# Kernel optimization log

Hardware: AMD Instinct MI355X
Metric: run time of the kernel (lower is better)

Reference implementation:

```python
import jax, jax.numpy as jnp
import numpy as np

N = 8192
D_IN = 60
NUM_CLASSES = 10


def _xavier(key, out_f, in_f):
    limit = float(np.sqrt(6.0 / (in_f + out_f)))
    return jax.random.uniform(key, (out_f, in_f), jnp.float32, -limit, limit)


def setup_inputs() -> dict:
    key = jax.random.key(0)
    ks = jax.random.split(key, 10)
    return {
        "x": jax.random.normal(ks[0], (N, D_IN), jnp.float32),
        "fc1_w": _xavier(ks[1], 32, 60),
        "fc1_b": jnp.zeros((32,), jnp.float32),
        "fc2_w": _xavier(ks[2], 16, 32),
        "fc2_b": jnp.zeros((16,), jnp.float32),
        "fc3_w": _xavier(ks[3], 8, 60),
        "fc3_b": jnp.zeros((8,), jnp.float32),
        "fc6_w": _xavier(ks[4], NUM_CLASSES, 8),
        "fc6_b": jnp.zeros((NUM_CLASSES,), jnp.float32),
        "temp": jnp.float32(1.0) + 0.1 * jax.random.truncated_normal(ks[5], -2.0, 2.0, (), jnp.float32),
        "theta": jnp.float32(1.0) + 0.1 * jax.random.truncated_normal(ks[6], -2.0, 2.0, (), jnp.float32),
    }


def _pairwise_sq_dist(z):
    # z: [N, d] -> [N, N] squared euclidean distances, clamped at 0
    sq = jnp.sum(z * z, axis=1)  # [N]
    dist = sq[:, None] + sq[None, :] - 2.0 * (z @ z.T)
    return jnp.maximum(dist, 0.0)


def reference(x, fc1_w, fc1_b, fc2_w, fc2_b, fc3_w, fc3_b, fc6_w, fc6_b, temp, theta):
    net = x @ fc1_w.T + fc1_b           # [N, 32]
    net = net @ fc2_w.T + fc2_b         # [N, 16]
    A = -_pairwise_sq_dist(net)         # [N, N]
    A = jax.nn.sigmoid(temp * A + theta)
    # A * (1 - I) + I == set diagonal to 1
    A = jnp.fill_diagonal(A, 1.0, inplace=False)
    A = A / jnp.sum(A, axis=1, keepdims=True)
    h = A @ x                           # [N, 60] dense graph aggregation
    h = h @ fc3_w.T + fc3_b             # [N, 8]
    return jax.nn.softmax(h @ fc6_w.T + fc6_b, axis=1)  # [N, num_classes]
```

## Files before the change

kernel.cpp:

```cpp
#include <hip/hip_runtime.h>
#include <math.h>

#define NROWS 8192
#define DIN   60
#define DZ    16
#define NC    10

#define LOG2E 1.4426950408889634f

#define RB      128
#define CJ      512
#define NRB     (NROWS / RB)
#define NCH     (NROWS / CJ)
#define WAVES   4
#define REGIONS (NRB * WAVES)

#define CHPAD (NROWS * 64 + 1024)

typedef short    bf16x8 __attribute__((ext_vector_type(8)));
typedef float    f32x4  __attribute__((ext_vector_type(4)));
typedef float    f32x16 __attribute__((ext_vector_type(16)));
typedef unsigned u32x2  __attribute__((ext_vector_type(2)));

__device__ __forceinline__ unsigned int bfr(float f) {
    return (__float_as_uint(f) + 0x8000u) >> 16;
}

__global__ __launch_bounds__(64) void k1_all(
    const float* __restrict__ x,
    const float* __restrict__ w1, const float* __restrict__ b1,
    const float* __restrict__ w2, const float* __restrict__ b2,
    const float* __restrict__ temp_p, const float* __restrict__ theta_p,
    unsigned short* __restrict__ zb, float* __restrict__ bbf,
    unsigned short* __restrict__ xT)
{
    int i = blockIdx.x * 64 + threadIdx.x;

    float xr[DIN];
    const float4* xp = reinterpret_cast<const float4*>(x + (size_t)i * DIN);
    #pragma unroll
    for (int c = 0; c < 15; ++c) {
        float4 v = xp[c];
        xr[c*4+0] = v.x; xr[c*4+1] = v.y; xr[c*4+2] = v.z; xr[c*4+3] = v.w;
    }

    float n1[32];
    #pragma unroll
    for (int o = 0; o < 32; ++o) {
        float acc = b1[o];
        #pragma unroll
        for (int k = 0; k < DIN; ++k) acc = fmaf(w1[o*DIN+k], xr[k], acc);
        n1[o] = acc;
    }

    float z[DZ];
    float sq = 0.0f;
    #pragma unroll
    for (int u = 0; u < DZ; ++u) {
        float acc = b2[u];
        #pragma unroll
        for (int o = 0; o < 32; ++o) acc = fmaf(w2[u*32+o], n1[o], acc);
        z[u] = acc;
        sq = fmaf(acc, acc, sq);
    }

    float temp  = *temp_p;
    float theta = *theta_p;
    float s = sqrtf(2.0f * temp * LOG2E);

    unsigned int p[8];
    #pragma unroll
    for (int u = 0; u < 8; ++u) {
        unsigned int lo = bfr(z[2*u]   * s);
        unsigned int hi = bfr(z[2*u+1] * s);
        p[u] = lo | (hi << 16);
    }
    uint4* dst = reinterpret_cast<uint4*>(zb + (size_t)i * 16);
    dst[0] = make_uint4(p[0], p[1], p[2], p[3]);
    dst[1] = make_uint4(p[4], p[5], p[6], p[7]);

    bbf[i] = LOG2E * fmaf(temp, sq, -0.5f * theta);

    #pragma unroll
    for (int c = 0; c < DIN; ++c)
        xT[(size_t)c * NROWS + i] = (unsigned short)bfr(xr[c]);
    xT[(size_t)60 * NROWS + i] = 0x3F80;
    xT[(size_t)61 * NROWS + i] = 0;
    xT[(size_t)62 * NROWS + i] = 0;
    xT[(size_t)63 * NROWS + i] = 0;
}

__global__ __launch_bounds__(256) void k2_mfma(
    const unsigned short* __restrict__ zb, const float* __restrict__ bbf,
    const unsigned short* __restrict__ xT, const float* __restrict__ theta_p,
    float* __restrict__ hacc)
{
    const int tid  = threadIdx.x;
    const int lane = tid & 63, wave = tid >> 6;
    const int ic = lane & 31;
    const int h  = lane >> 5;
    const int rb = blockIdx.x & (NRB - 1);
    const int ch = blockIdx.x >> 6;
    const int it = rb * RB + wave * 32;
    const int j0 = ch * CJ;

    bf16x8 zbi = *reinterpret_cast<const bf16x8*>(zb + (size_t)(it + ic) * 16 + h * 8);
    const float bi = bbf[it + ic];
    const float nclamp = -(*theta_p) * LOG2E;

    const int  dd   = ic - 4 * h;
    const bool dl   = (dd >= 0) && ((dd & 7) < 4);
    const int  dreg = dl ? (((dd >> 3) << 2) | (dd & 3)) : -1;

    f32x16 z16;
    #pragma unroll
    for (int k = 0; k < 16; ++k) z16[k] = 0.0f;
    f32x16 H0 = z16, H1 = z16;

    for (int jb = 0; jb < CJ / 32; ++jb) {
        const int jt = j0 + jb * 32;
        bf16x8 za = *reinterpret_cast<const bf16x8*>(zb + (size_t)(jt + ic) * 16 + h * 8);
        f32x16 S = __builtin_amdgcn_mfma_f32_32x32x16_bf16(za, zbi, z16, 0, 0, 0);

        const bool dblk = (it == jt);
        unsigned pk[8];
        #pragma unroll
        for (int u = 0; u < 4; ++u) {
            f32x4 bj = *reinterpret_cast<const f32x4*>(bbf + jt + u * 8 + 4 * h);
            unsigned ur[4];
            #pragma unroll
            for (int r = 0; r < 4; ++r) {
                const int reg = u * 4 + r;
                float n = (bi + bj[r]) - S[reg];
                n = fmaxf(n, nclamp);
                float P = __builtin_amdgcn_rcpf(1.0f + __builtin_amdgcn_exp2f(n));
                if (dblk && reg == dreg) P = 0.0f;
                ur[r] = __float_as_uint(P) + 0x8000u;
            }
            pk[u*2 + 0] = (ur[0] >> 16) | (ur[1] & 0xFFFF0000u);
            pk[u*2 + 1] = (ur[2] >> 16) | (ur[3] & 0xFFFF0000u);
        }

        u32x2 sA = __builtin_amdgcn_permlane32_swap(pk[0], pk[2], false, false);
        u32x2 sB = __builtin_amdgcn_permlane32_swap(pk[1], pk[3], false, false);
        u32x2 sC = __builtin_amdgcn_permlane32_swap(pk[4], pk[6], false, false);
        u32x2 sD = __builtin_amdgcn_permlane32_swap(pk[5], pk[7], false, false);
        union { unsigned u[4]; bf16x8 v; } pa0, pa1;
        pa0.u[0] = sA[0]; pa0.u[1] = sB[0]; pa0.u[2] = sA[1]; pa0.u[3] = sB[1];
        pa1.u[0] = sC[0]; pa1.u[1] = sD[0]; pa1.u[2] = sC[1]; pa1.u[3] = sD[1];

        {
            bf16x8 xb0 = *reinterpret_cast<const bf16x8*>(
                xT + (size_t)(ic) * NROWS + jt + h*8);
            bf16x8 xb1 = *reinterpret_cast<const bf16x8*>(
                xT + (size_t)(ic) * NROWS + jt + 16 + h*8);
            H0 = __builtin_amdgcn_mfma_f32_32x32x16_bf16(pa0.v, xb0, H0, 0, 0, 0);
            H0 = __builtin_amdgcn_mfma_f32_32x32x16_bf16(pa1.v, xb1, H0, 0, 0, 0);
        }
        {
            bf16x8 xb0 = *reinterpret_cast<const bf16x8*>(
                xT + (size_t)(32 + ic) * NROWS + jt + h*8);
            bf16x8 xb1 = *reinterpret_cast<const bf16x8*>(
                xT + (size_t)(32 + ic) * NROWS + jt + 16 + h*8);
            H1 = __builtin_amdgcn_mfma_f32_32x32x16_bf16(pa0.v, xb0, H1, 0, 0, 0);
            H1 = __builtin_amdgcn_mfma_f32_32x32x16_bf16(pa1.v, xb1, H1, 0, 0, 0);
        }
    }

    const int region = rb * WAVES + wave;
    float* outp = hacc + (size_t)ch * CHPAD + (size_t)region * 2048;
    #pragma unroll
    for (int reg = 0; reg < 16; ++reg)
        outp[reg * 64 + lane] = H0[reg];
    #pragma unroll
    for (int reg = 0; reg < 16; ++reg)
        outp[(16 + reg) * 64 + lane] = H1[reg];
}

__global__ __launch_bounds__(256) void k3_fused(
    const float* __restrict__ hacc,
    const float* __restrict__ x,
    const float* __restrict__ w3, const float* __restrict__ b3,
    const float* __restrict__ w6, const float* __restrict__ b6,
    float* __restrict__ out)
{
    __shared__ float sh[16][64];

    const int tid    = threadIdx.x;
    const int b      = blockIdx.x;
    const int region = b >> 1, sub = b & 1;

    {
        const int nt   = tid >> 7;
        const int foff = (tid & 127) * 4;
        const int rr   = foff >> 6;
        const int lane = foff & 63;
        const size_t base = (size_t)region * 2048 + nt * 1024 + sub * 512 + foff;

        float4 s = make_float4(0.0f, 0.0f, 0.0f, 0.0f);
        #pragma unroll 4
        for (int cc = 0; cc < NCH; ++cc) {
            int ch = (cc + b) & (NCH - 1);
            float4 v = *reinterpret_cast<const float4*>(
                hacc + (size_t)ch * CHPAD + base);
            s.x += v.x; s.y += v.y; s.z += v.z; s.w += v.w;
        }
        const int il  = (rr & 3) + 8 * (rr >> 2) + 4 * (lane >> 5);
        const int col = nt * 32 + (lane & 31);
        *reinterpret_cast<float4*>(&sh[il][col]) = s;
    }
    __syncthreads();

    if (tid < 16) {
        const int row = region * 32 + sub * 16 + tid;
        const float* hi = sh[tid];
        const float* xi = x + (size_t)row * DIN;

        float rd = __builtin_amdgcn_rcpf(hi[60] + 1.0f);

        float h[DIN];
        #pragma unroll
        for (int k = 0; k < DIN; ++k) h[k] = (hi[k] + xi[k]) * rd;

        float g[8];
        #pragma unroll
        for (int o = 0; o < 8; ++o) {
            float a = b3[o];
            #pragma unroll
            for (int k = 0; k < DIN; ++k) a = fmaf(w3[o*DIN+k], h[k], a);
            g[o] = a;
        }

        float l[NC];
        float m = -3.0e38f;
        #pragma unroll
        for (int c = 0; c < NC; ++c) {
            float a = b6[c];
            #pragma unroll
            for (int o = 0; o < 8; ++o) a = fmaf(w6[c*8+o], g[o], a);
            l[c] = a;
            m = fmaxf(m, a);
        }
        float e[NC];
        float sum = 0.0f;
        #pragma unroll
        for (int c = 0; c < NC; ++c) {
            e[c] = __builtin_amdgcn_exp2f((l[c] - m) * LOG2E);
            sum += e[c];
        }
        float rsum = __builtin_amdgcn_rcpf(sum);
        #pragma unroll
        for (int c = 0; c < NC; ++c) out[(size_t)row * NC + c] = e[c] * rsum;
    }
}

extern "C" void kernel_launch(void* const* d_in, const int* in_sizes, int n_in,
                              void* d_out, int out_size, void* d_ws, size_t ws_size,
                              hipStream_t stream)
{
    const float* x     = (const float*)d_in[0];
    const float* w1    = (const float*)d_in[1];
    const float* b1    = (const float*)d_in[2];
    const float* w2    = (const float*)d_in[3];
    const float* b2    = (const float*)d_in[4];
    const float* w3    = (const float*)d_in[5];
    const float* b3    = (const float*)d_in[6];
    const float* w6    = (const float*)d_in[7];
    const float* b6    = (const float*)d_in[8];
    const float* temp  = (const float*)d_in[9];
    const float* theta = (const float*)d_in[10];
    float* out = (float*)d_out;

    char* p = (char*)d_ws;
    unsigned short* zbuf = (unsigned short*)p;  p += (size_t)NROWS * 16 * 2;
    float*          bbf  = (float*)p;           p += (size_t)NROWS * 4;
    unsigned short* xT   = (unsigned short*)p;  p += (size_t)64 * NROWS * 2;
    float*          hacc = (float*)p;

    k1_all  <<<NROWS / 64, 64, 0, stream>>>(x, w1, b1, w2, b2, temp, theta, zbuf, bbf, xT);
    k2_mfma <<<NRB * NCH, 256, 0, stream>>>(zbuf, bbf, xT, theta, hacc);
    k3_fused<<<REGIONS * 2, 256, 0, stream>>>(hacc, x, w3, b3, w6, b6, out);
}
```

Measured before the change: 179.2 us.

## Replace per-chunk partial buffers with atomic accumulation into a single output buffer

k2 now reduces its 16 column-chunk partials with float atomic adds straight into one 8192x64 buffer, zeroed by a memset, instead of writing 16 separate partial slabs that k3 then summed. k3 becomes a simple per-row head kernel reading the finished sums. This removes about 32 MB of partial writes and reads plus the reduction pass. In exchange it adds atomic contention and a memset, and the summation order is no longer deterministic.

```diff
diff --git a/kernel.cpp b/kernel.cpp
--- a/kernel.cpp
+++ b/kernel.cpp
@@ -13,9 +13,6 @@
 #define NRB     (NROWS / RB)
 #define NCH     (NROWS / CJ)
 #define WAVES   4
-#define REGIONS (NRB * WAVES)
-
-#define CHPAD (NROWS * 64 + 1024)
 
 typedef short    bf16x8 __attribute__((ext_vector_type(8)));
 typedef float    f32x4  __attribute__((ext_vector_type(4)));
@@ -93,7 +90,7 @@
 __global__ __launch_bounds__(256) void k2_mfma(
     const unsigned short* __restrict__ zb, const float* __restrict__ bbf,
     const unsigned short* __restrict__ xT, const float* __restrict__ theta_p,
-    float* __restrict__ hacc)
+    float* __restrict__ hfin)
 {
     const int tid  = threadIdx.x;
     const int lane = tid & 63, wave = tid >> 6;
@@ -167,91 +164,61 @@
         }
     }
 
-    const int region = rb * WAVES + wave;
-    float* outp = hacc + (size_t)ch * CHPAD + (size_t)region * 2048;
-    #pragma unroll
-    for (int reg = 0; reg < 16; ++reg)
-        outp[reg * 64 + lane] = H0[reg];
-    #pragma unroll
-    for (int reg = 0; reg < 16; ++reg)
-        outp[(16 + reg) * 64 + lane] = H1[reg];
-}
-
-__global__ __launch_bounds__(256) void k3_fused(
-    const float* __restrict__ hacc,
+    #pragma unroll
+    for (int reg = 0; reg < 16; ++reg) {
+        const int row = it + (reg & 3) + 8 * (reg >> 2) + 4 * h;
+        unsafeAtomicAdd(hfin + (size_t)row * 64 + ic,      H0[reg]);
+        unsafeAtomicAdd(hfin + (size_t)row * 64 + 32 + ic, H1[reg]);
+    }
+}
+
+__global__ __launch_bounds__(64) void k3_head(
     const float* __restrict__ x,
     const float* __restrict__ w3, const float* __restrict__ b3,
     const float* __restrict__ w6, const float* __restrict__ b6,
+    const float* __restrict__ hfin,
     float* __restrict__ out)
 {
-    __shared__ float sh[16][64];
-
-    const int tid    = threadIdx.x;
-    const int b      = blockIdx.x;
-    const int region = b >> 1, sub = b & 1;
-
-    {
-        const int nt   = tid >> 7;
-        const int foff = (tid & 127) * 4;
-        const int rr   = foff >> 6;
-        const int lane = foff & 63;
-        const size_t base = (size_t)region * 2048 + nt * 1024 + sub * 512 + foff;
-
-        float4 s = make_float4(0.0f, 0.0f, 0.0f, 0.0f);
-        #pragma unroll 4
-        for (int cc = 0; cc < NCH; ++cc) {
-            int ch = (cc + b) & (NCH - 1);
-            float4 v = *reinterpret_cast<const float4*>(
-                hacc + (size_t)ch * CHPAD + base);
-            s.x += v.x; s.y += v.y; s.z += v.z; s.w += v.w;
-        }
-        const int il  = (rr & 3) + 8 * (rr >> 2) + 4 * (lane >> 5);
-        const int col = nt * 32 + (lane & 31);
-        *reinterpret_cast<float4*>(&sh[il][col]) = s;
-    }
-    __syncthreads();
-
-    if (tid < 16) {
-        const int row = region * 32 + sub * 16 + tid;
-        const float* hi = sh[tid];
-        const float* xi = x + (size_t)row * DIN;
-
-        float rd = __builtin_amdgcn_rcpf(hi[60] + 1.0f);
-
-        float h[DIN];
-        #pragma unroll
-        for (int k = 0; k < DIN; ++k) h[k] = (hi[k] + xi[k]) * rd;
-
-        float g[8];
-        #pragma unroll
-        for (int o = 0; o < 8; ++o) {
-            float a = b3[o];
-            #pragma unroll
-            for (int k = 0; k < DIN; ++k) a = fmaf(w3[o*DIN+k], h[k], a);
-            g[o] = a;
-        }
-
-        float l[NC];
-        float m = -3.0e38f;
-        #pragma unroll
-        for (int c = 0; c < NC; ++c) {
-            float a = b6[c];
-            #pragma unroll
-            for (int o = 0; o < 8; ++o) a = fmaf(w6[c*8+o], g[o], a);
-            l[c] = a;
-            m = fmaxf(m, a);
-        }
-        float e[NC];
-        float sum = 0.0f;
-        #pragma unroll
-        for (int c = 0; c < NC; ++c) {
-            e[c] = __builtin_amdgcn_exp2f((l[c] - m) * LOG2E);
-            sum += e[c];
-        }
-        float rsum = __builtin_amdgcn_rcpf(sum);
-        #pragma unroll
-        for (int c = 0; c < NC; ++c) out[(size_t)row * NC + c] = e[c] * rsum;
-    }
+    int i = blockIdx.x * 64 + threadIdx.x;
+
+    const float* hi = hfin + (size_t)i * 64;
+    const float* xi = x + (size_t)i * DIN;
+
+    float rd = __builtin_amdgcn_rcpf(hi[60] + 1.0f);
+
+    float h[DIN];
+    #pragma unroll
+    for (int k = 0; k < DIN; ++k) h[k] = (hi[k] + xi[k]) * rd;
+
+    float g[8];
+    #pragma unroll
+    for (int o = 0; o < 8; ++o) {
+        float a = b3[o];
+        #pragma unroll
+        for (int k = 0; k < DIN; ++k) a = fmaf(w3[o*DIN+k], h[k], a);
+        g[o] = a;
+    }
+
+    float l[NC];
+    float m = -3.0e38f;
+    #pragma unroll
+    for (int c = 0; c < NC; ++c) {
+        float a = b6[c];
+        #pragma unroll
+        for (int o = 0; o < 8; ++o) a = fmaf(w6[c*8+o], g[o], a);
+        l[c] = a;
+        m = fmaxf(m, a);
+    }
+    float e[NC];
+    float sum = 0.0f;
+    #pragma unroll
+    for (int c = 0; c < NC; ++c) {
+        e[c] = __builtin_amdgcn_exp2f((l[c] - m) * LOG2E);
+        sum += e[c];
+    }
+    float rsum = __builtin_amdgcn_rcpf(sum);
+    #pragma unroll
+    for (int c = 0; c < NC; ++c) out[(size_t)i * NC + c] = e[c] * rsum;
 }
 
 extern "C" void kernel_launch(void* const* d_in, const int* in_sizes, int n_in,
@@ -275,9 +242,10 @@
     unsigned short* zbuf = (unsigned short*)p;  p += (size_t)NROWS * 16 * 2;
     float*          bbf  = (float*)p;           p += (size_t)NROWS * 4;
     unsigned short* xT   = (unsigned short*)p;  p += (size_t)64 * NROWS * 2;
-    float*          hacc = (float*)p;
-
-    k1_all  <<<NROWS / 64, 64, 0, stream>>>(x, w1, b1, w2, b2, temp, theta, zbuf, bbf, xT);
-    k2_mfma <<<NRB * NCH, 256, 0, stream>>>(zbuf, bbf, xT, theta, hacc);
-    k3_fused<<<REGIONS * 2, 256, 0, stream>>>(hacc, x, w3, b3, w6, b6, out);
-}
+    float*          hfin = (float*)p;
+
+    hipMemsetAsync(hfin, 0, (size_t)NROWS * 64 * sizeof(float), stream);
+    k1_all <<<NROWS / 64, 64, 0, stream>>>(x, w1, b1, w2, b2, temp, theta, zbuf, bbf, xT);
+    k2_mfma<<<NRB * NCH, 256, 0, stream>>>(zbuf, bbf, xT, theta, hfin);
+    k3_head<<<NROWS / 64, 64, 0, stream>>>(x, w3, b3, w6, b6, hfin, out);
+}
```

After: 183.7 us. 2.5% more time.
